# Optimization experiments

Measured on AMD Instinct MI355X. Metric: run time of the kernel, lower is better.

## Reference

```python
import jax, jax.numpy as jnp
import numpy as np

B, D, C, K = 8192, 2048, 4096, 1000  # batch, input_dim, num_centers, num_classes


def setup_inputs() -> dict:
    key = jax.random.key(0)
    k0, k1, k2 = jax.random.split(key, 3)
    x = jax.random.normal(k0, (B, D), dtype=jnp.float32)
    centers = jax.random.normal(k1, (C, D), dtype=jnp.float32)
    beta = jnp.ones((C,), dtype=jnp.float32)
    W = jax.random.normal(k2, (K, C), dtype=jnp.float32) * 0.02  # fc.weight
    b = jnp.zeros((K,), dtype=jnp.float32)  # fc.bias
    return {"x": x, "centers": centers, "beta": beta, "W": W, "b": b}


def reference(x, centers, beta, W, b):
    # Pairwise Euclidean distance via the Gram trick (same math as
    # torch.norm(x[:,None,:] - centers, dim=2), without the (B,C,D) intermediate).
    x2 = jnp.sum(x * x, axis=-1, keepdims=True)          # (B, 1)
    c2 = jnp.sum(centers * centers, axis=-1)             # (C,)
    sq = x2 + c2[None, :] - 2.0 * (x @ centers.T)        # (B, C) squared distances
    dist = jnp.sqrt(jnp.maximum(sq, 0.0))
    act = jnp.exp(-beta[None, :] * dist)                 # RBF activations
    act = act / jnp.sum(act, axis=1, keepdims=True)      # normalize over centers
    return act @ W.T + b                                 # linear head (B, K)
```

## Files before the change

### kernel.cpp

```cpp
#include <hip/hip_runtime.h>


#define BB 8192
#define DD 2048
#define CC 4096
#define KK 1000
#define KP 1024

typedef unsigned short u16;
typedef __bf16 bf16x8 __attribute__((ext_vector_type(8)));
typedef float f32x16 __attribute__((ext_vector_type(16)));

typedef const void __attribute__((address_space(1)))* gvp_t;
typedef void __attribute__((address_space(3)))* lvp_t;

__device__ __forceinline__ u16 f2bf(float f) {
  union { float f; unsigned u; } v; v.f = f;
  return (u16)((v.u + 0x7fffu + ((v.u >> 16) & 1u)) >> 16);
}

__global__ void prep_norm_cast(const float* __restrict__ x, const float* __restrict__ cen,
                               u16* __restrict__ xb, u16* __restrict__ cb,
                               float* __restrict__ x2, float* __restrict__ c2) {
  int row = blockIdx.x;
  const float* src;
  u16* dst;
  float* nrm;
  if (row < BB) {
    src = x + (size_t)row * DD; dst = xb + (size_t)row * DD; nrm = x2 + row;
  } else {
    int r = row - BB;
    src = cen + (size_t)r * DD; dst = cb + (size_t)r * DD; nrm = c2 + r;
  }
  int t = threadIdx.x;
  float s = 0.f;
#pragma unroll
  for (int m = 0; m < 2; ++m) {
    int idx = t + 256 * m;
    float4 v = reinterpret_cast<const float4*>(src)[idx];
    s += v.x * v.x + v.y * v.y + v.z * v.z + v.w * v.w;
    reinterpret_cast<ushort4*>(dst)[idx] =
        make_ushort4(f2bf(v.x), f2bf(v.y), f2bf(v.z), f2bf(v.w));
  }
#pragma unroll
  for (int off = 1; off < 64; off <<= 1) s += __shfl_xor(s, off);
  __shared__ float red[4];
  if ((t & 63) == 0) red[t >> 6] = s;
  __syncthreads();
  if (t == 0) *nrm = red[0] + red[1] + red[2] + red[3];
}

__global__ void prep_wcast(const float* __restrict__ W, u16* __restrict__ wb) {
  int row = blockIdx.x;
  int t = threadIdx.x;
  ushort4* dst = reinterpret_cast<ushort4*>(wb + (size_t)row * CC);
  if (row < KK) {
    const float4* src = reinterpret_cast<const float4*>(W + (size_t)row * CC);
#pragma unroll
    for (int m = 0; m < 4; ++m) {
      float4 v = src[t + 256 * m];
      dst[t + 256 * m] = make_ushort4(f2bf(v.x), f2bf(v.y), f2bf(v.z), f2bf(v.w));
    }
  } else {
#pragma unroll
    for (int m = 0; m < 4; ++m) dst[t + 256 * m] = make_ushort4(0, 0, 0, 0);
  }
}

__global__ __launch_bounds__(256, 3)
void gemm1_rbf(const u16* __restrict__ Abf, const u16* __restrict__ Bbf,
               const float* __restrict__ x2, const float* __restrict__ c2,
               const float* __restrict__ beta, u16* __restrict__ Ebf) {
  constexpr int Kd = DD;
  __shared__ __align__(16) char smem[49152];

  const int t = threadIdx.x;
  const int lane = t & 63;
  const int wave = t >> 6;
  const int wr = wave >> 1, wc = wave & 1;
  const int l31 = lane & 31, khalf = lane >> 5;

  const int rowBase = blockIdx.y * 256;
  const int colBase = blockIdx.x * 128;

  f32x16 acc[4][2];
#pragma unroll
  for (int i = 0; i < 4; ++i)
#pragma unroll
    for (int j = 0; j < 2; ++j) acc[i][j] = 0.f;

  const int sr = t >> 3;
  const int fstage = ((t >> 3) & 7) ^ (((t >> 6) & 3) << 1);
  const int srcChunkOff = ((t & 7) ^ fstage) * 8;
  const u16* gA0 = Abf + (size_t)(rowBase + sr) * Kd + srcChunkOff;
  const u16* gB0 = Bbf + (size_t)(colBase + sr) * Kd + srcChunkOff;

  const int fv = (l31 & 7) ^ (((l31 >> 3) & 3) << 1);

  for (int kc = 0; kc < Kd; kc += 64) {
#pragma unroll
    for (int it = 0; it < 8; ++it) {
      const u16* ga = gA0 + (size_t)(32 * it) * Kd + kc;
      __builtin_amdgcn_global_load_lds((gvp_t)ga, (lvp_t)(smem + it * 4096 + t * 16), 16, 0, 0);
    }
#pragma unroll
    for (int it = 0; it < 4; ++it) {
      const u16* gb = gB0 + (size_t)(32 * it) * Kd + kc;
      __builtin_amdgcn_global_load_lds((gvp_t)gb, (lvp_t)(smem + 32768 + it * 4096 + t * 16), 16, 0, 0);
    }
    __syncthreads();
#pragma unroll
    for (int ks = 0; ks < 4; ++ks) {
      const int slot = ((ks * 2 + khalf) ^ fv) * 16;
      bf16x8 af[4], bfr[2];
#pragma unroll
      for (int i = 0; i < 4; ++i) {
        int r = wr * 128 + i * 32 + l31;
        af[i] = *(const bf16x8*)(smem + r * 128 + slot);
      }
#pragma unroll
      for (int j = 0; j < 2; ++j) {
        int r = wc * 64 + j * 32 + l31;
        bfr[j] = *(const bf16x8*)(smem + 32768 + r * 128 + slot);
      }
#pragma unroll
      for (int j = 0; j < 2; ++j)
#pragma unroll
        for (int i = 0; i < 4; ++i)
          acc[i][j] = __builtin_amdgcn_mfma_f32_32x32x16_bf16(af[i], bfr[j], acc[i][j], 0, 0, 0);
    }
    __syncthreads();
  }

  const int rbase = rowBase + wr * 128 + 4 * khalf;
  const int cbase = colBase + wc * 64;
  float c2v[2], bet[2];
  int gcol[2];
#pragma unroll
  for (int j = 0; j < 2; ++j) {
    gcol[j] = cbase + j * 32 + l31;
    c2v[j] = c2[gcol[j]];
    bet[j] = beta[gcol[j]];
  }
#pragma unroll
  for (int i = 0; i < 4; ++i) {
#pragma unroll
    for (int reg = 0; reg < 16; ++reg) {
      int grow = rbase + i * 32 + (reg & 3) + 8 * (reg >> 2);
      float x2v = x2[grow];
#pragma unroll
      for (int j = 0; j < 2; ++j) {
        float d = acc[i][j][reg];
        float sq = fmaxf(x2v + c2v[j] - 2.0f * d, 0.0f);
        float e = __expf(-bet[j] * __builtin_amdgcn_sqrtf(sq));
        Ebf[(size_t)grow * CC + gcol[j]] = f2bf(e);
      }
    }
  }
}

__global__ void rowsum_k(const u16* __restrict__ Ebf, float* __restrict__ rowsum) {
  const int lane = threadIdx.x & 63;
  const int row = blockIdx.x * 4 + (threadIdx.x >> 6);
  const uint4* p = reinterpret_cast<const uint4*>(Ebf + (size_t)row * CC);
  float s = 0.f;
#pragma unroll
  for (int it = 0; it < 8; ++it) {
    uint4 v = p[lane + 64 * it];
    unsigned w[4] = {v.x, v.y, v.z, v.w};
#pragma unroll
    for (int q = 0; q < 4; ++q) {
      union { unsigned u; float f; } lo, hi;
      lo.u = w[q] << 16;
      hi.u = w[q] & 0xffff0000u;
      s += lo.f + hi.f;
    }
  }
#pragma unroll
  for (int off = 1; off < 64; off <<= 1) s += __shfl_xor(s, off);
  if (lane == 0) rowsum[row] = s;
}

__global__ __launch_bounds__(256, 3)
void gemm2_out(const u16* __restrict__ Ebf, const u16* __restrict__ Wbf,
               const float* __restrict__ rowsum, const float* __restrict__ bias,
               float* __restrict__ out) {
  constexpr int Kd = CC;
  __shared__ __align__(16) char smem[32768];

  const int t = threadIdx.x;
  const int lane = t & 63;
  const int wave = t >> 6;
  const int wr = wave >> 1, wc = wave & 1;
  const int l31 = lane & 31, khalf = lane >> 5;

  const int rowBase = blockIdx.y * 128;
  const int colBase = blockIdx.x * 128;

  f32x16 acc[2][2];
#pragma unroll
  for (int i = 0; i < 2; ++i)
#pragma unroll
    for (int j = 0; j < 2; ++j) acc[i][j] = 0.f;

  const int sr = t >> 3;
  const int fstage = ((t >> 3) & 7) ^ (((t >> 6) & 3) << 1);
  const int srcChunkOff = ((t & 7) ^ fstage) * 8;
  const u16* gA0 = Ebf + (size_t)(rowBase + sr) * Kd + srcChunkOff;
  const u16* gB0 = Wbf + (size_t)(colBase + sr) * Kd + srcChunkOff;
  const int fv = (l31 & 7) ^ (((l31 >> 3) & 3) << 1);

  for (int kc = 0; kc < Kd; kc += 64) {
#pragma unroll
    for (int it = 0; it < 4; ++it) {
      const u16* ga = gA0 + (size_t)(32 * it) * Kd + kc;
      __builtin_amdgcn_global_load_lds((gvp_t)ga, (lvp_t)(smem + it * 4096 + t * 16), 16, 0, 0);
    }
#pragma unroll
    for (int it = 0; it < 4; ++it) {
      const u16* gb = gB0 + (size_t)(32 * it) * Kd + kc;
      __builtin_amdgcn_global_load_lds((gvp_t)gb, (lvp_t)(smem + 16384 + it * 4096 + t * 16), 16, 0, 0);
    }
    __syncthreads();
#pragma unroll
    for (int ks = 0; ks < 4; ++ks) {
      const int slot = ((ks * 2 + khalf) ^ fv) * 16;
      bf16x8 af[2], bfr[2];
#pragma unroll
      for (int i = 0; i < 2; ++i) {
        int r = wr * 64 + i * 32 + l31;
        af[i] = *(const bf16x8*)(smem + r * 128 + slot);
      }
#pragma unroll
      for (int j = 0; j < 2; ++j) {
        int r = wc * 64 + j * 32 + l31;
        bfr[j] = *(const bf16x8*)(smem + 16384 + r * 128 + slot);
      }
#pragma unroll
      for (int j = 0; j < 2; ++j)
#pragma unroll
        for (int i = 0; i < 2; ++i)
          acc[i][j] = __builtin_amdgcn_mfma_f32_32x32x16_bf16(af[i], bfr[j], acc[i][j], 0, 0, 0);
    }
    __syncthreads();
  }

  const int rbase = rowBase + wr * 64 + 4 * khalf;
  const int cbase = colBase + wc * 64;
  int gcol[2];
  float bv[2];
#pragma unroll
  for (int j = 0; j < 2; ++j) {
    gcol[j] = cbase + j * 32 + l31;
    bv[j] = (gcol[j] < KK) ? bias[gcol[j]] : 0.f;
  }
#pragma unroll
  for (int i = 0; i < 2; ++i) {
#pragma unroll
    for (int reg = 0; reg < 16; ++reg) {
      int grow = rbase + i * 32 + (reg & 3) + 8 * (reg >> 2);
      float inv = 1.0f / rowsum[grow];
#pragma unroll
      for (int j = 0; j < 2; ++j) {
        if (gcol[j] < KK)
          out[(size_t)grow * KK + gcol[j]] = acc[i][j][reg] * inv + bv[j];
      }
    }
  }
}

#define OFF_XB 0u
#define OFF_CB 33554432u
#define OFF_WB 50331648u
#define OFF_EB 58720256u
#define OFF_X2 125829120u
#define OFF_C2 125861888u
#define OFF_RS 125878272u

extern "C" void kernel_launch(void* const* d_in, const int* in_sizes, int n_in,
                              void* d_out, int out_size, void* d_ws, size_t ws_size,
                              hipStream_t stream) {
  const float* x = (const float*)d_in[0];
  const float* cen = (const float*)d_in[1];
  const float* beta = (const float*)d_in[2];
  const float* W = (const float*)d_in[3];
  const float* bias = (const float*)d_in[4];
  float* out = (float*)d_out;
  char* ws = (char*)d_ws;

  u16* xb = (u16*)(ws + OFF_XB);
  u16* cb = (u16*)(ws + OFF_CB);
  u16* wb = (u16*)(ws + OFF_WB);
  u16* eb = (u16*)(ws + OFF_EB);
  float* x2 = (float*)(ws + OFF_X2);
  float* c2 = (float*)(ws + OFF_C2);
  float* rowsum = (float*)(ws + OFF_RS);

  prep_norm_cast<<<BB + CC, 256, 0, stream>>>(x, cen, xb, cb, x2, c2);
  prep_wcast<<<KP, 256, 0, stream>>>(W, wb);
  gemm1_rbf<<<dim3(CC / 128, BB / 256), 256, 0, stream>>>(xb, cb, x2, c2, beta, eb);
  rowsum_k<<<BB / 4, 256, 0, stream>>>(eb, rowsum);
  gemm2_out<<<dim3(KP / 128, BB / 128), 256, 0, stream>>>(eb, wb, rowsum, bias, out);
}
```

Before: 385.6 us.

## Rewrite distance GEMM as double-buffered 256x256 tile pipeline with 16x16 MFMA

The first GEMM moves from a 256x128 tile with 4 waves and a single LDS buffer to a 256x256 tile with 8 waves. It uses 128KB of double-buffered LDS and explicit interleaving of async global-to-LDS loads with MFMA quarters, controlled by sched_barrier, setprio and manual waitcnt. The inner product switches to 16x16x32 bf16 MFMA with a new XOR swizzle. The goal is to hide global load latency behind compute and double data reuse per block. The cost is higher LDS and register pressure, lower occupancy, and fragile manual synchronisation.

```diff
diff --git a/kernel.cpp b/kernel.cpp
--- a/kernel.cpp
+++ b/kernel.cpp
@@ -9,6 +9,7 @@
 
 typedef unsigned short u16;
 typedef __bf16 bf16x8 __attribute__((ext_vector_type(8)));
+typedef float f32x4 __attribute__((ext_vector_type(4)));
 typedef float f32x16 __attribute__((ext_vector_type(16)));
 
 typedef const void __attribute__((address_space(1)))* gvp_t;
@@ -67,93 +68,151 @@
   }
 }
 
-__global__ __launch_bounds__(256, 3)
+
+#define SB0 __builtin_amdgcn_sched_barrier(0)
+#define BARR __builtin_amdgcn_s_barrier()
+#define LGKM0 asm volatile("s_waitcnt lgkmcnt(0)" ::: "memory")
+
+#define ST_A(BUF, H, TILE)                                                         \
+  {                                                                                \
+    const u16* _s = gA0 + (size_t)((H) * 128) * DD + (TILE) * 64;                  \
+    char* _d = (char*)smem + (BUF) * 65536 + (H) * 16384 + t * 16;                 \
+    __builtin_amdgcn_global_load_lds((gvp_t)_s, (lvp_t)_d, 16, 0, 0);              \
+    __builtin_amdgcn_global_load_lds((gvp_t)(_s + (size_t)64 * DD),                \
+                                     (lvp_t)(_d + 8192), 16, 0, 0);                \
+  }
+
+#define ST_B(BUF, H, TILE)                                                         \
+  {                                                                                \
+    const u16* _s = gB0 + (size_t)((H) * 128) * DD + (TILE) * 64;                  \
+    char* _d = (char*)smem + (BUF) * 65536 + 32768 + (H) * 16384 + t * 16;         \
+    __builtin_amdgcn_global_load_lds((gvp_t)_s, (lvp_t)_d, 16, 0, 0);              \
+    __builtin_amdgcn_global_load_lds((gvp_t)(_s + (size_t)64 * DD),                \
+                                     (lvp_t)(_d + 8192), 16, 0, 0);                \
+  }
+
+#define READ_B(SBP)                                                                \
+  _Pragma("unroll") for (int n_ = 0; n_ < 4; ++n_) {                               \
+    _Pragma("unroll") for (int ks_ = 0; ks_ < 2; ++ks_) {                          \
+      bfr[n_][ks_] = *(const bf16x8*)((SBP) + bRow + n_ * 2048 + cbv[ks_]);        \
+    }                                                                              \
+  }
+
+#define READ_A(SAP, MQ)                                                            \
+  _Pragma("unroll") for (int m_ = 0; m_ < 2; ++m_) {                               \
+    _Pragma("unroll") for (int ks_ = 0; ks_ < 2; ++ks_) {                          \
+      af[m_][ks_] =                                                                \
+          *(const bf16x8*)((SAP) + aRow + ((MQ)*2 + m_) * 2048 + cbv[ks_]);        \
+    }                                                                              \
+  }
+
+#define MFMA_Q(MQ)                                                                 \
+  __builtin_amdgcn_s_setprio(1);                                                   \
+  _Pragma("unroll") for (int m_ = 0; m_ < 2; ++m_) {                               \
+    _Pragma("unroll") for (int n_ = 0; n_ < 4; ++n_) {                             \
+      _Pragma("unroll") for (int ks_ = 0; ks_ < 2; ++ks_) {                        \
+        acc[(MQ)*2 + m_][n_] = __builtin_amdgcn_mfma_f32_16x16x32_bf16(            \
+            af[m_][ks_], bfr[n_][ks_], acc[(MQ)*2 + m_][n_], 0, 0, 0);             \
+      }                                                                            \
+    }                                                                              \
+  }                                                                                \
+  __builtin_amdgcn_s_setprio(0)
+
+#define TILE_BODY(TILE, CUR, DOA, DOB, VMN)                                        \
+  {                                                                                \
+    const char* sA_ = (const char*)smem + (CUR) * 65536;                           \
+    const char* sB_ = sA_ + 32768;                                                 \
+    READ_B(sB_);                                                                   \
+    READ_A(sA_, 0);                                                                \
+    SB0;                                                                           \
+    if (DOA) { ST_A(1 - (CUR), 0, (TILE) + 1); ST_A(1 - (CUR), 1, (TILE) + 1); }   \
+    SB0; BARR; LGKM0; SB0;                                                         \
+    MFMA_Q(0); SB0; BARR;                                                          \
+    READ_A(sA_, 1); SB0;                                                           \
+    if (DOB) { ST_B((CUR), 0, (TILE) + 2); }                                       \
+    SB0; BARR; LGKM0; SB0;                                                         \
+    MFMA_Q(1); SB0; BARR;                                                          \
+    READ_A(sA_, 2); SB0;                                                           \
+    if (DOB) { ST_B((CUR), 1, (TILE) + 2); }                                       \
+    SB0; BARR; LGKM0; SB0;                                                         \
+    MFMA_Q(2); SB0; BARR;                                                          \
+    READ_A(sA_, 3); SB0; BARR; LGKM0; SB0;                                         \
+    MFMA_Q(3);                                                                     \
+    if ((VMN) == 4) { asm volatile("s_waitcnt vmcnt(4)" ::: "memory"); }           \
+    else if ((VMN) == 0) { asm volatile("s_waitcnt vmcnt(0)" ::: "memory"); }      \
+    SB0; BARR;                                                                     \
+  }
+
+__global__ __launch_bounds__(512, 2)
 void gemm1_rbf(const u16* __restrict__ Abf, const u16* __restrict__ Bbf,
                const float* __restrict__ x2, const float* __restrict__ c2,
                const float* __restrict__ beta, u16* __restrict__ Ebf) {
-  constexpr int Kd = DD;
-  __shared__ __align__(16) char smem[49152];
+  constexpr int NT = DD / 64;
+  __shared__ __align__(16) char smem[131072];
 
   const int t = threadIdx.x;
   const int lane = t & 63;
   const int wave = t >> 6;
-  const int wr = wave >> 1, wc = wave & 1;
-  const int l31 = lane & 31, khalf = lane >> 5;
+  const int wr = wave >> 2;
+  const int wc = wave & 3;
+  const int l15 = lane & 15;
 
   const int rowBase = blockIdx.y * 256;
-  const int colBase = blockIdx.x * 128;
-
-  f32x16 acc[4][2];
-#pragma unroll
-  for (int i = 0; i < 4; ++i)
-#pragma unroll
-    for (int j = 0; j < 2; ++j) acc[i][j] = 0.f;
-
-  const int sr = t >> 3;
-  const int fstage = ((t >> 3) & 7) ^ (((t >> 6) & 3) << 1);
-  const int srcChunkOff = ((t & 7) ^ fstage) * 8;
-  const u16* gA0 = Abf + (size_t)(rowBase + sr) * Kd + srcChunkOff;
-  const u16* gB0 = Bbf + (size_t)(colBase + sr) * Kd + srcChunkOff;
-
-  const int fv = (l31 & 7) ^ (((l31 >> 3) & 3) << 1);
-
-  for (int kc = 0; kc < Kd; kc += 64) {
-#pragma unroll
-    for (int it = 0; it < 8; ++it) {
-      const u16* ga = gA0 + (size_t)(32 * it) * Kd + kc;
-      __builtin_amdgcn_global_load_lds((gvp_t)ga, (lvp_t)(smem + it * 4096 + t * 16), 16, 0, 0);
-    }
-#pragma unroll
-    for (int it = 0; it < 4; ++it) {
-      const u16* gb = gB0 + (size_t)(32 * it) * Kd + kc;
-      __builtin_amdgcn_global_load_lds((gvp_t)gb, (lvp_t)(smem + 32768 + it * 4096 + t * 16), 16, 0, 0);
-    }
-    __syncthreads();
-#pragma unroll
-    for (int ks = 0; ks < 4; ++ks) {
-      const int slot = ((ks * 2 + khalf) ^ fv) * 16;
-      bf16x8 af[4], bfr[2];
-#pragma unroll
-      for (int i = 0; i < 4; ++i) {
-        int r = wr * 128 + i * 32 + l31;
-        af[i] = *(const bf16x8*)(smem + r * 128 + slot);
-      }
-#pragma unroll
-      for (int j = 0; j < 2; ++j) {
-        int r = wc * 64 + j * 32 + l31;
-        bfr[j] = *(const bf16x8*)(smem + 32768 + r * 128 + slot);
-      }
-#pragma unroll
-      for (int j = 0; j < 2; ++j)
-#pragma unroll
-        for (int i = 0; i < 4; ++i)
-          acc[i][j] = __builtin_amdgcn_mfma_f32_32x32x16_bf16(af[i], bfr[j], acc[i][j], 0, 0, 0);
-    }
-    __syncthreads();
-  }
-
-  const int rbase = rowBase + wr * 128 + 4 * khalf;
-  const int cbase = colBase + wc * 64;
-  float c2v[2], bet[2];
-  int gcol[2];
-#pragma unroll
-  for (int j = 0; j < 2; ++j) {
-    gcol[j] = cbase + j * 32 + l31;
-    c2v[j] = c2[gcol[j]];
-    bet[j] = beta[gcol[j]];
-  }
-#pragma unroll
-  for (int i = 0; i < 4; ++i) {
-#pragma unroll
-    for (int reg = 0; reg < 16; ++reg) {
-      int grow = rbase + i * 32 + (reg & 3) + 8 * (reg >> 2);
-      float x2v = x2[grow];
-#pragma unroll
-      for (int j = 0; j < 2; ++j) {
-        float d = acc[i][j][reg];
-        float sq = fmaxf(x2v + c2v[j] - 2.0f * d, 0.0f);
-        float e = __expf(-bet[j] * __builtin_amdgcn_sqrtf(sq));
-        Ebf[(size_t)grow * CC + gcol[j]] = f2bf(e);
+  const int colBase = blockIdx.x * 256;
+
+  f32x4 acc[8][4];
+#pragma unroll
+  for (int i = 0; i < 8; ++i)
+#pragma unroll
+    for (int j = 0; j < 4; ++j) acc[i][j] = 0.f;
+
+  const int srow = t >> 3;
+  const u16* gA0 = Abf + (size_t)(rowBase + srow) * DD + ((t & 7) ^ (srow & 7)) * 8;
+  const u16* gB0 = Bbf + (size_t)(colBase + srow) * DD + ((t & 7) ^ (srow & 7)) * 8;
+
+  int cbv[2];
+  cbv[0] = (((lane >> 4) & 3) ^ (lane & 7)) << 4;
+  cbv[1] = ((4 + ((lane >> 4) & 3)) ^ (lane & 7)) << 4;
+  const int aRow = (wr * 128 + l15) * 128;
+  const int bRow = (wc * 64 + l15) * 128;
+
+  bf16x8 bfr[4][2];
+  bf16x8 af[2][2];
+
+  ST_A(0, 0, 0); ST_A(0, 1, 0); ST_B(0, 0, 0); ST_B(0, 1, 0);
+  ST_B(1, 0, 1); ST_B(1, 1, 1);
+  asm volatile("s_waitcnt vmcnt(4)" ::: "memory");
+  BARR;
+
+#pragma unroll 2
+  for (int tile = 0; tile < NT - 2; ++tile) {
+    TILE_BODY(tile, tile & 1, true, true, 4);
+  }
+  TILE_BODY(NT - 2, (NT - 2) & 1, true, false, 0);
+  TILE_BODY(NT - 1, (NT - 1) & 1, false, false, -1);
+
+  const int khi4 = (lane >> 4) * 4;
+  float c2v[4], bet[4];
+  int gc[4];
+#pragma unroll
+  for (int n = 0; n < 4; ++n) {
+    gc[n] = colBase + wc * 64 + n * 16 + l15;
+    c2v[n] = c2[gc[n]];
+    bet[n] = beta[gc[n]];
+  }
+#pragma unroll
+  for (int m = 0; m < 8; ++m) {
+#pragma unroll
+    for (int r = 0; r < 4; ++r) {
+      const int grow = rowBase + wr * 128 + m * 16 + khi4 + r;
+      const float x2v = x2[grow];
+      u16* orow = Ebf + (size_t)grow * CC;
+#pragma unroll
+      for (int n = 0; n < 4; ++n) {
+        float d = acc[m][n][r];
+        float sq = fmaxf(x2v + c2v[n] - 2.0f * d, 0.0f);
+        float e = __expf(-bet[n] * __builtin_amdgcn_sqrtf(sq));
+        orow[gc[n]] = f2bf(e);
       }
     }
   }
@@ -225,22 +284,22 @@
 #pragma unroll
     for (int ks = 0; ks < 4; ++ks) {
       const int slot = ((ks * 2 + khalf) ^ fv) * 16;
-      bf16x8 af[2], bfr[2];
+      bf16x8 af2[2], bfr2[2];
 #pragma unroll
       for (int i = 0; i < 2; ++i) {
         int r = wr * 64 + i * 32 + l31;
-        af[i] = *(const bf16x8*)(smem + r * 128 + slot);
+        af2[i] = *(const bf16x8*)(smem + r * 128 + slot);
       }
 #pragma unroll
       for (int j = 0; j < 2; ++j) {
         int r = wc * 64 + j * 32 + l31;
-        bfr[j] = *(const bf16x8*)(smem + 16384 + r * 128 + slot);
+        bfr2[j] = *(const bf16x8*)(smem + 16384 + r * 128 + slot);
       }
 #pragma unroll
       for (int j = 0; j < 2; ++j)
 #pragma unroll
         for (int i = 0; i < 2; ++i)
-          acc[i][j] = __builtin_amdgcn_mfma_f32_32x32x16_bf16(af[i], bfr[j], acc[i][j], 0, 0, 0);
+          acc[i][j] = __builtin_amdgcn_mfma_f32_32x32x16_bf16(af2[i], bfr2[j], acc[i][j], 0, 0, 0);
     }
     __syncthreads();
   }
@@ -298,7 +357,7 @@
 
   prep_norm_cast<<<BB + CC, 256, 0, stream>>>(x, cen, xb, cb, x2, c2);
   prep_wcast<<<KP, 256, 0, stream>>>(W, wb);
-  gemm1_rbf<<<dim3(CC / 128, BB / 256), 256, 0, stream>>>(xb, cb, x2, c2, beta, eb);
+  gemm1_rbf<<<dim3(CC / 256, BB / 256), 512, 0, stream>>>(xb, cb, x2, c2, beta, eb);
   rowsum_k<<<BB / 4, 256, 0, stream>>>(eb, rowsum);
   gemm2_out<<<dim3(KP / 128, BB / 128), 256, 0, stream>>>(eb, wb, rowsum, bias, out);
 }
```

Result: faster. 367.6 us (-4.7%).
